# Performance work log

Measured on AMD Instinct MI355X. Metric: run time of the kernel, lower is better.

Reference implementation:

```python
import jax, jax.numpy as jnp
import numpy as np

B, D, N_LABELS = 8192, 512, 256

def setup_inputs() -> dict:
    key = jax.random.key(0)
    kz, km = jax.random.split(key)
    z = jax.random.normal(kz, (B, D), dtype=jnp.float32)
    Mx = jax.random.randint(km, (B,), 0, N_LABELS, dtype=jnp.int64)
    return {"z": z, "Mx": Mx}

def reference(z, Mx):
    # Mx: [B] int labels -> equality mask [B, B] with zero diagonal
    Mx2 = Mx.reshape(-1, 1)  # [B, 1]
    mask_Mx = (Mx2 == Mx2.T).astype(z.dtype)
    mask_Mx = mask_Mx * (1.0 - jnp.eye(z.shape[0], dtype=z.dtype))
    # pairwise L2 distances (cdist p=2) via gram trick, grad-safe sqrt
    sq = jnp.sum(z * z, axis=-1)                      # [B]
    d2 = sq[:, None] + sq[None, :] - 2.0 * (z @ z.T)  # [B, B]
    pos = d2 > 0.0
    dist = jnp.sqrt(jnp.where(pos, d2, 1.0)) * pos.astype(z.dtype)
    n_select = mask_Mx.sum(axis=1)                    # [B]
    valid = n_select > 0
    row_sum = (mask_Mx * dist).sum(axis=1)
    # torch masked_select drops rows with no positives; with these label
    # stats every row has positives, so returning the full [B] vector
    # (zeros where invalid) matches the selected result.
    loss = jnp.where(valid, row_sum / jnp.maximum(n_select, 1.0), 0.0)
    return loss
```

## Files before the change

### kernel.cpp

```cpp
#include <hip/hip_runtime.h>
#include <math.h>

#define B_ROWS 8192
#define D_DIM 512
#define N_LABELS 256
#define GMAX 64
#define THREADS 1024
#define WAVES 16
#define SEG (B_ROWS / WAVES)
#define SITER (SEG / 64)
#define LSTRIDE (D_DIM + 8)

typedef __attribute__((ext_vector_type(8))) short bf16x8;
typedef __attribute__((ext_vector_type(4))) float f32x4;

static __device__ __forceinline__ unsigned int f2bf(float f) {
    unsigned int u = __float_as_uint(f);
    return (u + 0x7FFFu + ((u >> 16) & 1u)) >> 16;
}
static __device__ __forceinline__ float bfval(unsigned int b) {
    return __uint_as_float(b << 16);
}

__global__ __launch_bounds__(THREADS) void loss_kernel(const float* __restrict__ z,
                                                       const int* __restrict__ Mx,
                                                       float* __restrict__ out) {
    __shared__ __align__(16) unsigned short hi_sh[GMAX][LSTRIDE];
    __shared__ __align__(16) unsigned short lo_sh[GMAX][LSTRIDE];
    __shared__ int   ids_sh[GMAX];
    __shared__ float sq_sh[GMAX];
    __shared__ float rowpart[WAVES][GMAX];
    __shared__ unsigned long long msk_sh[WAVES][SITER];
    __shared__ int   wcnt[WAVES], wbase[WAVES];
    __shared__ int   cnt_sh;

    const int lbl  = blockIdx.x;
    const int tid  = threadIdx.x;
    const int wv   = tid >> 6;
    const int lane = tid & 63;
    const int sb   = wv * SEG;

    int c = 0;
    #pragma unroll
    for (int t = 0; t < SITER; ++t) {
        const bool m = (Mx[sb + t * 64 + lane] == lbl);
        const unsigned long long bal = __ballot(m);
        if (lane == 0) msk_sh[wv][t] = bal;
        c += __popcll(bal);
    }
    if (lane == 0) wcnt[wv] = c;
    __syncthreads();
    if (tid == 0) {
        int b = 0;
        #pragma unroll
        for (int w = 0; w < WAVES; ++w) { wbase[w] = b; b += wcnt[w]; }
        cnt_sh = b;
    }
    __syncthreads();
    const int cnt = cnt_sh;
    if (cnt <= 0) return;

    if (cnt > GMAX) {
        int k = 0;
        for (int i = 0; i < B_ROWS; ++i) {
            if (Mx[i] != lbl) continue;
            if ((k++ % WAVES) != wv) continue;
            float acc = 0.f;
            for (int j = 0; j < B_ROWS; ++j) {
                if (Mx[j] != lbl || j == i) continue;
                float s = 0.f;
                for (int d = lane; d < D_DIM; d += 64) {
                    const float t = z[(size_t)i * D_DIM + d] - z[(size_t)j * D_DIM + d];
                    s = fmaf(t, t, s);
                }
                s += __shfl_xor(s, 1, 64);
                s += __shfl_xor(s, 2, 64);
                s += __shfl_xor(s, 4, 64);
                s += __shfl_xor(s, 8, 64);
                s += __shfl_xor(s, 16, 64);
                s += __shfl_xor(s, 32, 64);
                acc += (s > 0.f) ? sqrtf(s) : 0.f;
            }
            if (lane == 0) out[i] = acc / (float)(cnt - 1);
        }
        return;
    }

    {
        int pos = wbase[wv];
        const unsigned long long lower = (lane == 0) ? 0ull : ((1ull << lane) - 1ull);
        #pragma unroll
        for (int t = 0; t < SITER; ++t) {
            const unsigned long long bal = msk_sh[wv][t];
            if ((bal >> lane) & 1ull)
                ids_sh[pos + __popcll(bal & lower)] = sb + t * 64 + lane;
            pos += __popcll(bal);
        }
    }
    for (int i = tid; i < WAVES * GMAX; i += THREADS) ((float*)rowpart)[i] = 0.f;
    __syncthreads();

    for (int c2 = tid; c2 < cnt * (D_DIM / 4); c2 += THREADS) {
        const int row = c2 >> 7;
        const int c4  = c2 & 127;
        const float4 v = *(const float4*)(z + (size_t)ids_sh[row] * D_DIM + c4 * 4);
        const unsigned int h0 = f2bf(v.x), h1 = f2bf(v.y), h2 = f2bf(v.z), h3 = f2bf(v.w);
        const unsigned int g0 = f2bf(v.x - bfval(h0));
        const unsigned int g1 = f2bf(v.y - bfval(h1));
        const unsigned int g2 = f2bf(v.z - bfval(h2));
        const unsigned int g3 = f2bf(v.w - bfval(h3));
        *(uint2*)&hi_sh[row][c4 * 4] = make_uint2(h0 | (h1 << 16), h2 | (h3 << 16));
        *(uint2*)&lo_sh[row][c4 * 4] = make_uint2(g0 | (g1 << 16), g2 | (g3 << 16));
    }
    __syncthreads();

    const int NT = (cnt + 15) >> 4;
    const int TS = NT * (NT + 1) / 2;

    int jt = 0;
    #pragma unroll
    for (int q = 1; q < 4; ++q) jt += (wv >= q * (q + 1) / 2);
    const int it = wv - jt * (jt + 1) / 2;
    const bool own = (wv < TS);

    const int l15 = lane & 15;
    const int lh  = lane >> 4;

    f32x4 acc = {0.f, 0.f, 0.f, 0.f};
    if (own) {
        #pragma unroll
        for (int k4 = 0; k4 < D_DIM / 32; ++k4) {
            const int kb = k4 * 32 + lh * 8;
            const bf16x8 ah = *(const bf16x8*)&hi_sh[it * 16 + l15][kb];
            const bf16x8 al = *(const bf16x8*)&lo_sh[it * 16 + l15][kb];
            const bf16x8 bh = *(const bf16x8*)&hi_sh[jt * 16 + l15][kb];
            const bf16x8 bl = *(const bf16x8*)&lo_sh[jt * 16 + l15][kb];
            acc = __builtin_amdgcn_mfma_f32_16x16x32_bf16(ah, bh, acc, 0, 0, 0);
            acc = __builtin_amdgcn_mfma_f32_16x16x32_bf16(ah, bl, acc, 0, 0, 0);
            acc = __builtin_amdgcn_mfma_f32_16x16x32_bf16(al, bh, acc, 0, 0, 0);
        }
    }

    if (own && it == jt) {
        #pragma unroll
        for (int r = 0; r < 4; ++r) {
            const int drow = lh * 4 + r;
            if (l15 == drow) sq_sh[it * 16 + drow] = acc[r];
        }
    }
    __syncthreads();

    if (own) {
        float d0 = 0.f, d1 = 0.f, d2v = 0.f, d3 = 0.f;
        #pragma unroll
        for (int r = 0; r < 4; ++r) {
            const int gi = it * 16 + lh * 4 + r;
            const int gj = jt * 16 + l15;
            const float d2 = sq_sh[gi] + sq_sh[gj] - 2.f * acc[r];
            const bool valid = (gi < cnt) && (gj < cnt) && (gi != gj) && (d2 > 0.f);
            const float dist = valid ? sqrtf(d2) : 0.f;
            if (r == 0) d0 = dist; else if (r == 1) d1 = dist; else if (r == 2) d2v = dist; else d3 = dist;

            float rs = dist;
            rs += __shfl_xor(rs, 1, 64);
            rs += __shfl_xor(rs, 2, 64);
            rs += __shfl_xor(rs, 4, 64);
            rs += __shfl_xor(rs, 8, 64);
            if (l15 == 0) rowpart[wv][gi] += rs;
        }
        if (it != jt) {
            float cs = (d0 + d1) + (d2v + d3);
            cs += __shfl_xor(cs, 16, 64);
            cs += __shfl_xor(cs, 32, 64);
            if (lane < 16) rowpart[wv][jt * 16 + l15] += cs;
        }
    }
    __syncthreads();

    if (tid < cnt) {
        float s = 0.f;
        #pragma unroll
        for (int w = 0; w < WAVES; ++w) s += rowpart[w][tid];
        out[ids_sh[tid]] = (cnt > 1) ? s / (float)(cnt - 1) : 0.f;
    }
}

extern "C" void kernel_launch(void* const* d_in, const int* in_sizes, int n_in,
                              void* d_out, int out_size, void* d_ws, size_t ws_size,
                              hipStream_t stream) {
    const float* z  = (const float*)d_in[0];
    const int*   Mx = (const int*)d_in[1];
    float*       out = (float*)d_out;

    loss_kernel<<<N_LABELS, THREADS, 0, stream>>>(z, Mx, out);
}
```

Before: 13.25 us.

## Replace split-bf16 triple MFMA with single fp16 MFMA and wave-scan prefix

Drops the bf16 hi/lo split that took three MFMAs per k-step and stores each row once as fp16, issuing one f16 MFMA per k-step. This cuts the conversion work, the shared-memory footprint and traffic, and the matrix-core instructions. The serial prefix sum over per-wave counts is also replaced by a shuffle-based scan in wave 0. fp16 has fewer mantissa bits than the hi/lo pair, so the Gram matrix, and the distances taken by cancellation from it, lose accuracy.

```diff
diff --git a/kernel.cpp b/kernel.cpp
--- a/kernel.cpp
+++ b/kernel.cpp
@@ -11,22 +11,18 @@
 #define SITER (SEG / 64)
 #define LSTRIDE (D_DIM + 8)
 
-typedef __attribute__((ext_vector_type(8))) short bf16x8;
+typedef __attribute__((ext_vector_type(8))) _Float16 f16x8;
 typedef __attribute__((ext_vector_type(4))) float f32x4;
 
-static __device__ __forceinline__ unsigned int f2bf(float f) {
-    unsigned int u = __float_as_uint(f);
-    return (u + 0x7FFFu + ((u >> 16) & 1u)) >> 16;
-}
-static __device__ __forceinline__ float bfval(unsigned int b) {
-    return __uint_as_float(b << 16);
+static __device__ __forceinline__ unsigned short f2h(float f) {
+    const _Float16 h = (_Float16)f;
+    return __builtin_bit_cast(unsigned short, h);
 }
 
 __global__ __launch_bounds__(THREADS) void loss_kernel(const float* __restrict__ z,
                                                        const int* __restrict__ Mx,
                                                        float* __restrict__ out) {
-    __shared__ __align__(16) unsigned short hi_sh[GMAX][LSTRIDE];
-    __shared__ __align__(16) unsigned short lo_sh[GMAX][LSTRIDE];
+    __shared__ __align__(16) unsigned short h_sh[GMAX][LSTRIDE];
     __shared__ int   ids_sh[GMAX];
     __shared__ float sq_sh[GMAX];
     __shared__ float rowpart[WAVES][GMAX];
@@ -50,11 +46,16 @@
     }
     if (lane == 0) wcnt[wv] = c;
     __syncthreads();
-    if (tid == 0) {
-        int b = 0;
+
+    if (wv == 0) {
+        int v = (lane < WAVES) ? wcnt[lane] : 0;
         #pragma unroll
-        for (int w = 0; w < WAVES; ++w) { wbase[w] = b; b += wcnt[w]; }
-        cnt_sh = b;
+        for (int d = 1; d < WAVES; d <<= 1) {
+            const int o = __shfl_up(v, d, 64);
+            if (lane >= d) v += o;
+        }
+        if (lane < WAVES) wbase[lane] = v - wcnt[lane];
+        if (lane == WAVES - 1) cnt_sh = v;
     }
     __syncthreads();
     const int cnt = cnt_sh;
@@ -104,13 +105,9 @@
         const int row = c2 >> 7;
         const int c4  = c2 & 127;
         const float4 v = *(const float4*)(z + (size_t)ids_sh[row] * D_DIM + c4 * 4);
-        const unsigned int h0 = f2bf(v.x), h1 = f2bf(v.y), h2 = f2bf(v.z), h3 = f2bf(v.w);
-        const unsigned int g0 = f2bf(v.x - bfval(h0));
-        const unsigned int g1 = f2bf(v.y - bfval(h1));
-        const unsigned int g2 = f2bf(v.z - bfval(h2));
-        const unsigned int g3 = f2bf(v.w - bfval(h3));
-        *(uint2*)&hi_sh[row][c4 * 4] = make_uint2(h0 | (h1 << 16), h2 | (h3 << 16));
-        *(uint2*)&lo_sh[row][c4 * 4] = make_uint2(g0 | (g1 << 16), g2 | (g3 << 16));
+        const unsigned int p0 = (unsigned int)f2h(v.x) | ((unsigned int)f2h(v.y) << 16);
+        const unsigned int p1 = (unsigned int)f2h(v.z) | ((unsigned int)f2h(v.w) << 16);
+        *(uint2*)&h_sh[row][c4 * 4] = make_uint2(p0, p1);
     }
     __syncthreads();
 
@@ -131,13 +128,9 @@
         #pragma unroll
         for (int k4 = 0; k4 < D_DIM / 32; ++k4) {
             const int kb = k4 * 32 + lh * 8;
-            const bf16x8 ah = *(const bf16x8*)&hi_sh[it * 16 + l15][kb];
-            const bf16x8 al = *(const bf16x8*)&lo_sh[it * 16 + l15][kb];
-            const bf16x8 bh = *(const bf16x8*)&hi_sh[jt * 16 + l15][kb];
-            const bf16x8 bl = *(const bf16x8*)&lo_sh[jt * 16 + l15][kb];
-            acc = __builtin_amdgcn_mfma_f32_16x16x32_bf16(ah, bh, acc, 0, 0, 0);
-            acc = __builtin_amdgcn_mfma_f32_16x16x32_bf16(ah, bl, acc, 0, 0, 0);
-            acc = __builtin_amdgcn_mfma_f32_16x16x32_bf16(al, bh, acc, 0, 0, 0);
+            const f16x8 a = *(const f16x8*)&h_sh[it * 16 + l15][kb];
+            const f16x8 b = *(const f16x8*)&h_sh[jt * 16 + l15][kb];
+            acc = __builtin_amdgcn_mfma_f32_16x16x32_f16(a, b, acc, 0, 0, 0);
         }
     }
 
```

Result: faster. 12.94 us (-2.3%).
